# Optimization experiments

Measured on AMD Instinct MI355X. Metric: run time of the kernel, lower is better.

Reference implementation:

```python
import jax, jax.numpy as jnp
import numpy as np

B, N, C, O = 8, 4096, 256, 256  # batch, nodes, in_channels, out_channels
DENSITY = 0.01


def _cheb_k2(x_flat, A, W0, W1, b):
    """PyG ChebConv with K=2, sym normalization, lambda_max=2.
    Scaled Laplacian reduces to Lhat = -D^{-1/2} A D^{-1/2} (self-loops removed,
    diagonal of I - Ahat cancels with the fill_value=-1 self loops).
    Only the first N flattened nodes have edges (faithful to the source bug)."""
    n = A.shape[0]
    A = A * (1.0 - jnp.eye(n, dtype=A.dtype))  # remove_self_loops
    deg = A.sum(axis=1)                         # scatter(edge_weight, row)
    dis = jnp.where(deg > 0, jax.lax.rsqrt(jnp.where(deg > 0, deg, 1.0)), 0.0)
    Ahat = (dis[:, None] * A) * dis[None, :]    # D^{-1/2} A D^{-1/2}
    out = x_flat @ W0                           # Tx_0 term, all B*N nodes
    prop = -(Ahat @ x_flat[:n])                 # Tx_1 = Lhat x, first N nodes only
    out = out.at[:n].add(prop @ W1)
    return out + b


def setup_inputs() -> dict:
    key = jax.random.key(0)
    ks = jax.random.split(key, 12)
    x = jax.random.normal(ks[0], (B, N, C), jnp.float32)

    def adj(k):
        u = jax.random.uniform(k, (N, N), jnp.float32)
        return jnp.where(u < DENSITY, u, 0.0)

    adj1 = adj(ks[1])
    adj2 = adj(ks[2])
    s = 0.02
    Wc0_a = jax.random.normal(ks[3], (C, O), jnp.float32) * s
    Wc1_a = jax.random.normal(ks[4], (C, O), jnp.float32) * s
    bc_a = jnp.zeros((O,), jnp.float32)
    Wc0_b = jax.random.normal(ks[5], (C, O), jnp.float32) * s
    Wc1_b = jax.random.normal(ks[6], (C, O), jnp.float32) * s
    bc_b = jnp.zeros((O,), jnp.float32)
    Wp = jax.random.normal(ks[7], (2 * O, O), jnp.float32) * s  # [in,out] layout
    bp = jnp.zeros((O,), jnp.float32)
    return {"x": x, "adj1": adj1, "adj2": adj2,
            "Wc0_a": Wc0_a, "Wc1_a": Wc1_a, "bc_a": bc_a,
            "Wc0_b": Wc0_b, "Wc1_b": Wc1_b, "bc_b": bc_b,
            "Wp": Wp, "bp": bp}


def reference(x, adj1, adj2, Wc0_a, Wc1_a, bc_a, Wc0_b, Wc1_b, bc_b, Wp, bp):
    b, n, c = x.shape
    x_flat = x.reshape(-1, c)  # [B*N, C]
    o1 = _cheb_k2(x_flat, adj1, Wc0_a, Wc1_a, bc_a).reshape(b, n, -1)
    o2 = _cheb_k2(x_flat, adj2, Wc0_b, Wc1_b, bc_b).reshape(b, n, -1)
    out = jnp.concatenate([o1, o2], axis=-1)  # [B, N, 2*O]
    out = out @ Wp + bp                        # projection (dropout p=0)
    return out
```

## Files before the change

kernel.cpp:

```cpp
#include <hip/hip_runtime.h>
#include <hip/hip_bf16.h>
#include <stdint.h>

typedef __bf16 bf16;
typedef __attribute__((ext_vector_type(8))) __bf16 bf16x8;
typedef __attribute__((ext_vector_type(4))) float f32x4;


#define RCAP 96

__global__ __launch_bounds__(256) void k_prep(const float* __restrict__ adj1,
                                              const float* __restrict__ adj2,
                                              float* __restrict__ dis,
                                              int* __restrict__ ccnt,
                                              unsigned short* __restrict__ cidx,
                                              float* __restrict__ cval) {
  __shared__ int s_cnt;
  __shared__ float wsum[4];
  int t = threadIdx.x;
  int lane = t & 63, wave = t >> 6;
  int row = blockIdx.x;
  int which = blockIdx.y;
  const float* A = which ? adj2 : adj1;
  if (t == 0) s_cnt = 0;
  __syncthreads();
  const f32x4* Arow = (const f32x4*)(A + (size_t)row * 4096);
  int r = (which << 12) | row;
  size_t base = (size_t)r * RCAP;
  float s = 0.f;
#pragma unroll
  for (int it = 0; it < 4; ++it) {
    int idx4 = it * 256 + t;
    f32x4 v = Arow[idx4];
    int j0 = idx4 * 4;
#pragma unroll
    for (int k = 0; k < 4; ++k) {
      float f = v[k];
      int j = j0 + k;
      if (j != row) {
        s += f;
        if (f != 0.f) {
          int pos = atomicAdd(&s_cnt, 1);
          if (pos < RCAP) {
            cidx[base + pos] = (unsigned short)j;
            cval[base + pos] = f;
          }
        }
      }
    }
  }
#pragma unroll
  for (int off = 32; off >= 1; off >>= 1) s += __shfl_down(s, off, 64);
  if (lane == 0) wsum[wave] = s;
  __syncthreads();
  if (t == 0) {
    float tot = wsum[0] + wsum[1] + wsum[2] + wsum[3];
    dis[r] = (tot > 0.f) ? (1.0f / sqrtf(tot)) : 0.f;
    int n = s_cnt;
    ccnt[r] = (n > RCAP) ? RCAP : n;
  }
}

__global__ __launch_bounds__(256) void k_spmm2(const float* __restrict__ x,
                                               const float* __restrict__ dis,
                                               const int* __restrict__ ccnt,
                                               const unsigned short* __restrict__ cidx,
                                               const float* __restrict__ cval,
                                               bf16* __restrict__ P) {
  __shared__ float s_val[RCAP];
  __shared__ int s_idx[RCAP];
  int t = threadIdx.x;
  int row = blockIdx.x;
  int which = blockIdx.y;
  int r = (which << 12) | row;
  const float* dsel = dis + (which << 12);
  int n = ccnt[r];
  size_t base = (size_t)r * RCAP;
  if (t < n) {
    int j = cidx[base + t];
    s_idx[t] = j;
    s_val[t] = cval[base + t] * dsel[j];
  }
  __syncthreads();
  float acc = 0.f;
  int e = 0;
  for (; e + 4 <= n; e += 4) {
    float v0 = x[(size_t)s_idx[e + 0] * 256 + t];
    float v1 = x[(size_t)s_idx[e + 1] * 256 + t];
    float v2 = x[(size_t)s_idx[e + 2] * 256 + t];
    float v3 = x[(size_t)s_idx[e + 3] * 256 + t];
    acc += s_val[e + 0] * v0 + s_val[e + 1] * v1 + s_val[e + 2] * v2 + s_val[e + 3] * v3;
  }
  for (; e < n; ++e) acc += s_val[e] * x[(size_t)s_idx[e] * 256 + t];
  float prop = -dsel[row] * acc;
  P[(size_t)row * 512 + (size_t)which * 256 + t] = (bf16)prop;
}

__global__ __launch_bounds__(1024) void k_wprep(const float* __restrict__ W0a,
                                                const float* __restrict__ W1a,
                                                const float* __restrict__ bca,
                                                const float* __restrict__ W0b,
                                                const float* __restrict__ W1b,
                                                const float* __restrict__ bcb,
                                                const float* __restrict__ Wp,
                                                const float* __restrict__ bp,
                                                bf16* __restrict__ WxT,
                                                bf16* __restrict__ WextT,
                                                float* __restrict__ biasv) {
  __shared__ float red0[4][256], red1[4][256], red2[4][256], red3[4][256];
  int tid = threadIdx.x;
  int o = tid & 255;
  int ch = tid >> 8;
  int c = blockIdx.x;
  const float* r0a = W0a + (size_t)c * 256;
  const float* r0b = W0b + (size_t)c * 256;
  const float* r1a = W1a + (size_t)c * 256;
  const float* r1b = W1b + (size_t)c * 256;
  float ax = 0.f, a1 = 0.f, a2 = 0.f, bacc = 0.f;
#pragma unroll 8
  for (int mm = 0; mm < 64; ++mm) {
    int m = ch * 64 + mm;
    float wpt = Wp[(size_t)m * 256 + o];
    float wpb = Wp[(size_t)(m + 256) * 256 + o];
    float wa = r0a[m], wb = r0b[m];
    float w1 = r1a[m], w2 = r1b[m];
    ax += wa * wpt + wb * wpb;
    a1 += w1 * wpt;
    a2 += w2 * wpb;
    bacc += bca[m] * wpt + bcb[m] * wpb;
  }
  red0[ch][o] = ax; red1[ch][o] = a1; red2[ch][o] = a2; red3[ch][o] = bacc;
  __syncthreads();
  if (ch == 0) {
    ax = red0[0][o] + red0[1][o] + red0[2][o] + red0[3][o];
    a1 = red1[0][o] + red1[1][o] + red1[2][o] + red1[3][o];
    a2 = red2[0][o] + red2[1][o] + red2[2][o] + red2[3][o];
    bacc = red3[0][o] + red3[1][o] + red3[2][o] + red3[3][o];
    WxT[(size_t)o * 256 + c] = (bf16)ax;
    WextT[(size_t)o * 512 + c] = (bf16)a1;
    WextT[(size_t)o * 512 + 256 + c] = (bf16)a2;
    if (c == 0) biasv[o] = bacc + bp[o];
  }
}

__device__ __forceinline__ void mfma_tile(const char* ldsA, const char* ldsB,
                                          int wm, int wn, int lr, int quad,
                                          f32x4 acc[4][4]) {
  bf16x8 af[4], bb[4];
#pragma unroll
  for (int mf = 0; mf < 4; ++mf)
    af[mf] = *(const bf16x8*)(ldsA + ((wm * 64 + mf * 16 + lr) * 64 + quad * 16));
#pragma unroll
  for (int nf = 0; nf < 4; ++nf)
    bb[nf] = *(const bf16x8*)(ldsB + ((wn * 64 + nf * 16 + lr) * 64 + quad * 16));
#pragma unroll
  for (int mf = 0; mf < 4; ++mf)
#pragma unroll
    for (int nf = 0; nf < 4; ++nf)
      acc[mf][nf] = __builtin_amdgcn_mfma_f32_16x16x32_bf16(af[mf], bb[nf], acc[mf][nf], 0, 0, 0);
}

__global__ __launch_bounds__(256, 2) void k_gemm(const float* __restrict__ X,
                                                 const bf16* __restrict__ P,
                                                 const bf16* __restrict__ WxT,
                                                 const bf16* __restrict__ WextT,
                                                 const float* __restrict__ biasv,
                                                 float* __restrict__ out) {
  __shared__ __attribute__((aligned(16))) char ldsA[8192];
  __shared__ __attribute__((aligned(16))) char ldsB[8192];
  int t = threadIdx.x;
  int lane = t & 63, wave = t >> 6;
  int wm = wave & 1, wn = wave >> 1;
  int lr = lane & 15, quad = lane >> 4;
  int R0 = blockIdx.y * 128;
  int N0 = blockIdx.x * 128;

  f32x4 acc[4][4];
#pragma unroll
  for (int i = 0; i < 4; ++i)
#pragma unroll
    for (int j = 0; j < 4; ++j) acc[i][j] = (f32x4){0.f, 0.f, 0.f, 0.f};

  int srow = t >> 2;
  int scol = (t & 3) * 8;

#pragma unroll 1
  for (int step = 0; step < 8; ++step) {
    int kb = step * 32;
    const float* xp0 = X + (size_t)(R0 + srow) * 256 + kb + scol;
    const float* xp1 = X + (size_t)(R0 + srow + 64) * 256 + kb + scol;
    f32x4 f00 = *(const f32x4*)(xp0), f01 = *(const f32x4*)(xp0 + 4);
    f32x4 f10 = *(const f32x4*)(xp1), f11 = *(const f32x4*)(xp1 + 4);
    bf16x8 a0, a1;
#pragma unroll
    for (int k = 0; k < 4; ++k) {
      a0[k] = (bf16)f00[k]; a0[k + 4] = (bf16)f01[k];
      a1[k] = (bf16)f10[k]; a1[k + 4] = (bf16)f11[k];
    }
    bf16x8 b0 = *(const bf16x8*)(WxT + (size_t)(N0 + srow) * 256 + kb + scol);
    bf16x8 b1 = *(const bf16x8*)(WxT + (size_t)(N0 + srow + 64) * 256 + kb + scol);
    __syncthreads();
    *(bf16x8*)(ldsA + t * 16) = a0;
    *(bf16x8*)(ldsA + 4096 + t * 16) = a1;
    *(bf16x8*)(ldsB + t * 16) = b0;
    *(bf16x8*)(ldsB + 4096 + t * 16) = b1;
    __syncthreads();
    mfma_tile(ldsA, ldsB, wm, wn, lr, quad, acc);
  }

  if (R0 < 4096) {
#pragma unroll 1
    for (int step = 0; step < 16; ++step) {
      int kb = step * 32;
      bf16x8 a0 = *(const bf16x8*)(P + (size_t)(R0 + srow) * 512 + kb + scol);
      bf16x8 a1 = *(const bf16x8*)(P + (size_t)(R0 + srow + 64) * 512 + kb + scol);
      bf16x8 b0 = *(const bf16x8*)(WextT + (size_t)(N0 + srow) * 512 + kb + scol);
      bf16x8 b1 = *(const bf16x8*)(WextT + (size_t)(N0 + srow + 64) * 512 + kb + scol);
      __syncthreads();
      *(bf16x8*)(ldsA + t * 16) = a0;
      *(bf16x8*)(ldsA + 4096 + t * 16) = a1;
      *(bf16x8*)(ldsB + t * 16) = b0;
      *(bf16x8*)(ldsB + 4096 + t * 16) = b1;
      __syncthreads();
      mfma_tile(ldsA, ldsB, wm, wn, lr, quad, acc);
    }
  }

#pragma unroll
  for (int nf = 0; nf < 4; ++nf) {
    int ocol = N0 + wn * 64 + nf * 16 + lr;
    float bv = biasv[ocol];
#pragma unroll
    for (int mf = 0; mf < 4; ++mf) {
      int orow = R0 + wm * 64 + mf * 16 + quad * 4;
#pragma unroll
      for (int r = 0; r < 4; ++r)
        out[(size_t)(orow + r) * 256 + ocol] = acc[mf][nf][r] + bv;
    }
  }
}

extern "C" void kernel_launch(void* const* d_in, const int* in_sizes, int n_in,
                              void* d_out, int out_size, void* d_ws, size_t ws_size,
                              hipStream_t stream) {
  const float* x    = (const float*)d_in[0];
  const float* adj1 = (const float*)d_in[1];
  const float* adj2 = (const float*)d_in[2];
  const float* W0a  = (const float*)d_in[3];
  const float* W1a  = (const float*)d_in[4];
  const float* bca  = (const float*)d_in[5];
  const float* W0b  = (const float*)d_in[6];
  const float* W1b  = (const float*)d_in[7];
  const float* bcb  = (const float*)d_in[8];
  const float* Wp   = (const float*)d_in[9];
  const float* bp   = (const float*)d_in[10];
  float* out = (float*)d_out;

  char* ws = (char*)d_ws;
  float* dis   = (float*)(ws);
  float* biasv = (float*)(ws + 32 * 1024);
  bf16*  WxT   = (bf16*)(ws + 64 * 1024);
  bf16*  WextT = (bf16*)(ws + 320 * 1024);
  bf16*  P     = (bf16*)(ws + 704 * 1024);
  int*   ccnt  = (int*)(ws + 4800 * 1024);
  float* cval  = (float*)(ws + 4832 * 1024);
  unsigned short* cidx = (unsigned short*)(ws + 7904 * 1024);

  k_prep<<<dim3(4096, 2), dim3(256), 0, stream>>>(adj1, adj2, dis, ccnt, cidx, cval);
  k_wprep<<<dim3(256), dim3(1024), 0, stream>>>(W0a, W1a, bca, W0b, W1b, bcb, Wp, bp,
                                                WxT, WextT, biasv);
  k_spmm2<<<dim3(4096, 2), dim3(256), 0, stream>>>(x, dis, ccnt, cidx, cval, P);
  k_gemm<<<dim3(2, 256), dim3(256), 0, stream>>>(x, P, WxT, WextT, biasv, out);
}
```

Baseline: 256.6 us.

## Compact adjacency rows per wavefront with ballot prefix and remap GEMM row tiles

The prep kernel now gives each adjacency row to a single wavefront instead of a 256-thread block. It replaces the shared-memory atomic counter and block barriers with a ballot/popcount prefix compaction, which also keeps column order deterministic. The GEMM kernel also permutes its row-tile index so that consecutive blocks touch rows spread across the batch, which may change cache and channel behaviour. The prep grid shrinks to 2048 blocks of four waves, so each wave walks 16 vector loads serially.

```diff
diff --git a/kernel.cpp b/kernel.cpp
--- a/kernel.cpp
+++ b/kernel.cpp
@@ -15,49 +15,43 @@
                                               int* __restrict__ ccnt,
                                               unsigned short* __restrict__ cidx,
                                               float* __restrict__ cval) {
-  __shared__ int s_cnt;
-  __shared__ float wsum[4];
   int t = threadIdx.x;
-  int lane = t & 63, wave = t >> 6;
-  int row = blockIdx.x;
-  int which = blockIdx.y;
+  int wave = t >> 6, lane = t & 63;
+  int gw = blockIdx.x * 4 + wave;
+  int which = gw >> 12;
+  int row = gw & 4095;
   const float* A = which ? adj2 : adj1;
-  if (t == 0) s_cnt = 0;
-  __syncthreads();
   const f32x4* Arow = (const f32x4*)(A + (size_t)row * 4096);
-  int r = (which << 12) | row;
-  size_t base = (size_t)r * RCAP;
+  size_t base = (size_t)gw * RCAP;
+  unsigned long long lmask = (1ULL << lane) - 1ULL;
   float s = 0.f;
-#pragma unroll
-  for (int it = 0; it < 4; ++it) {
-    int idx4 = it * 256 + t;
-    f32x4 v = Arow[idx4];
-    int j0 = idx4 * 4;
+  int cnt = 0;
+#pragma unroll 4
+  for (int it = 0; it < 16; ++it) {
+    f32x4 v = Arow[it * 64 + lane];
+    int j0 = it * 256 + lane * 4;
 #pragma unroll
     for (int k = 0; k < 4; ++k) {
       float f = v[k];
       int j = j0 + k;
-      if (j != row) {
-        s += f;
-        if (f != 0.f) {
-          int pos = atomicAdd(&s_cnt, 1);
-          if (pos < RCAP) {
-            cidx[base + pos] = (unsigned short)j;
-            cval[base + pos] = f;
-          }
+      bool keep = (f != 0.f) && (j != row);
+      if (j != row) s += f;
+      unsigned long long bm = __ballot(keep);
+      if (keep) {
+        int pos = cnt + __popcll(bm & lmask);
+        if (pos < RCAP) {
+          cidx[base + pos] = (unsigned short)j;
+          cval[base + pos] = f;
         }
       }
+      cnt += (int)__popcll(bm);
     }
   }
 #pragma unroll
   for (int off = 32; off >= 1; off >>= 1) s += __shfl_down(s, off, 64);
-  if (lane == 0) wsum[wave] = s;
-  __syncthreads();
-  if (t == 0) {
-    float tot = wsum[0] + wsum[1] + wsum[2] + wsum[3];
-    dis[r] = (tot > 0.f) ? (1.0f / sqrtf(tot)) : 0.f;
-    int n = s_cnt;
-    ccnt[r] = (n > RCAP) ? RCAP : n;
+  if (lane == 0) {
+    dis[gw] = (s > 0.f) ? (1.0f / sqrtf(s)) : 0.f;
+    ccnt[gw] = (cnt > RCAP) ? RCAP : cnt;
   }
 }
 
@@ -172,7 +166,9 @@
   int lane = t & 63, wave = t >> 6;
   int wm = wave & 1, wn = wave >> 1;
   int lr = lane & 15, quad = lane >> 4;
-  int R0 = blockIdx.y * 128;
+  int yy = blockIdx.y;
+  int my = ((yy & 3) << 6) | (yy >> 2);
+  int R0 = my * 128;
   int N0 = blockIdx.x * 128;
 
   f32x4 acc[4][4];
@@ -266,7 +262,7 @@
   float* cval  = (float*)(ws + 4832 * 1024);
   unsigned short* cidx = (unsigned short*)(ws + 7904 * 1024);
 
-  k_prep<<<dim3(4096, 2), dim3(256), 0, stream>>>(adj1, adj2, dis, ccnt, cidx, cval);
+  k_prep<<<dim3(2048), dim3(256), 0, stream>>>(adj1, adj2, dis, ccnt, cidx, cval);
   k_wprep<<<dim3(256), dim3(1024), 0, stream>>>(W0a, W1a, bca, W0b, W1b, bcb, Wp, bp,
                                                 WxT, WextT, biasv);
   k_spmm2<<<dim3(4096, 2), dim3(256), 0, stream>>>(x, dis, ccnt, cidx, cval, P);
```

New measurement: 261.4 us. About the same (+1.9%).
